# Kernel tuning notes

Hardware: AMD Instinct MI355X
Metric: run time of the kernel (lower is better)

## Reference

```python
import jax, jax.numpy as jnp
import numpy as np

B, C_IN, C_OUT, T, R, CO = 8, 64, 64, 32, 32, 32


def setup_inputs() -> dict:
    key = jax.random.key(0)
    ks = jax.random.split(key, 8)
    scale = 1.0 / np.sqrt(C_IN)  # nn.Linear default uniform(-1/sqrt(in), 1/sqrt(in))
    w = lambda k: jax.random.uniform(k, (C_OUT, C_IN), jnp.float32, -scale, scale)
    return {
        "x": jax.random.normal(ks[0], (B, C_IN, T, R, CO), jnp.float32),
        "w_self": w(ks[1]),
        "w_tp": w(ks[2]),
        "w_tm": w(ks[3]),
        "w_rp": w(ks[4]),
        "w_rm": w(ks[5]),
        "w_cp": w(ks[6]),
        "w_cm": w(ks[7]),
    }


def _proj(v, w):
    # v: [B, t, r, c, C_in], w: [C_out, C_in] (nn.Linear layout)
    return jnp.einsum('btrci,oi->btrco', v, w)


def _shift_pad(a, axis, front):
    # pad 1 slice at front (True) or back (False) along `axis` of a 5-D tensor
    pads = [(0, 0)] * 5
    pads[axis] = (1, 0) if front else (0, 1)
    return jnp.pad(a, pads)


def reference(x, w_self, w_tp, w_tm, w_rp, w_rm, w_cp, w_cm):
    xp = jnp.transpose(x, (0, 2, 3, 4, 1))  # [B, T, R, Co, C_in]
    out = _proj(xp, w_self)
    if xp.shape[1] > 1:
        out = out + _shift_pad(_proj(xp[:, :-1], w_tp), 1, True)
        out = out + _shift_pad(_proj(xp[:, 1:], w_tm), 1, False)
    if xp.shape[2] > 1:
        out = out + _shift_pad(_proj(xp[:, :, :-1], w_rp), 2, True)
        out = out + _shift_pad(_proj(xp[:, :, 1:], w_rm), 2, False)
    if xp.shape[3] > 1:
        out = out + _shift_pad(_proj(xp[:, :, :, :-1], w_cp), 3, True)
        out = out + _shift_pad(_proj(xp[:, :, :, 1:], w_cm), 3, False)
    return jnp.transpose(out, (0, 4, 1, 2, 3))  # [B, C_out, T, R, Co]
```

## Files before the change

### kernel.cpp

```cpp
#include <hip/hip_runtime.h>


#define SB 32768
#define CIN 64
#define COUT 64
#define NB 8

typedef short s16x8 __attribute__((ext_vector_type(8)));
typedef __bf16 bf16x8 __attribute__((ext_vector_type(8)));
typedef float f32x4 __attribute__((ext_vector_type(4)));

__device__ __forceinline__ unsigned f2bf(float f) {
    unsigned u = __float_as_uint(f);
    u += 0x7FFFu + ((u >> 16) & 1u);
    return u >> 16;
}
__device__ __forceinline__ unsigned pk2(float lo, float hi) {
    return f2bf(lo) | (f2bf(hi) << 16);
}

__device__ __forceinline__ void gload_lds16(const void* g, void* l) {
    __builtin_amdgcn_global_load_lds(
        (const __attribute__((address_space(1))) void*)g,
        (__attribute__((address_space(3))) void*)l, 16, 0, 0);
}

__global__ __launch_bounds__(256) void wprep_kernel(const float* __restrict__ w0,
                            const float* __restrict__ w1, const float* __restrict__ w2,
                            const float* __restrict__ w3, const float* __restrict__ w4,
                            const float* __restrict__ w5, const float* __restrict__ w6,
                            unsigned short* __restrict__ ws) {
    int tap = blockIdx.x;
    int tid = threadIdx.x;
    const float* w = (tap == 0) ? w0 : (tap == 1) ? w1 : (tap == 2) ? w2
                   : (tap == 3) ? w3 : (tap == 4) ? w4 : (tap == 5) ? w5 : w6;
    unsigned p[8];
#pragma unroll
    for (int j = 0; j < 8; ++j)
        p[j] = pk2(w[tid * 16 + 2 * j], w[tid * 16 + 2 * j + 1]);
    uint4* dp = (uint4*)(ws + tap * 4096 + tid * 16);
    dp[0] = make_uint4(p[0], p[1], p[2], p[3]);
    dp[1] = make_uint4(p[4], p[5], p[6], p[7]);
}

__global__ __launch_bounds__(256) void prep2_kernel(const float* __restrict__ x,
                            const float* __restrict__ w0, const float* __restrict__ w1,
                            const float* __restrict__ w2, const float* __restrict__ w3,
                            const float* __restrict__ w4, const float* __restrict__ w5,
                            const float* __restrict__ w6,
                            unsigned short* __restrict__ ws) {
    int bid = blockIdx.x;
    int tid = threadIdx.x;
    if (bid >= 4096) {
        int tap = bid - 4096;
        const float* w = (tap == 0) ? w0 : (tap == 1) ? w1 : (tap == 2) ? w2
                       : (tap == 3) ? w3 : (tap == 4) ? w4 : (tap == 5) ? w5 : w6;
        unsigned p[8];
#pragma unroll
        for (int j = 0; j < 8; ++j)
            p[j] = pk2(w[tid * 16 + 2 * j], w[tid * 16 + 2 * j + 1]);
        uint4* dp = (uint4*)(ws + tap * 4096 + tid * 16);
        dp[0] = make_uint4(p[0], p[1], p[2], p[3]);
        dp[1] = make_uint4(p[4], p[5], p[6], p[7]);
        return;
    }
    int lbid = ((bid & 7) << 9) | (bid >> 3);
    int b = lbid >> 9;
    int i = (lbid & 511) * 256 + tid;
    int cg = i & 7;
    int s = (i >> 3) * 2;
    const float* xb = x + (size_t)b * CIN * SB;
    unsigned short* xq = ws + 7 * 4096;
    unsigned pa[4], pb[4];
#pragma unroll
    for (int u = 0; u < 4; ++u) {
        int ch = cg * 8 + 2 * u;
        float2 v0 = *(const float2*)(xb + (size_t)ch * SB + s);
        float2 v1 = *(const float2*)(xb + (size_t)(ch + 1) * SB + s);
        pa[u] = pk2(v0.x, v1.x);
        pb[u] = pk2(v0.y, v1.y);
    }
    uint4* dst = (uint4*)(xq + ((size_t)b * SB + s) * 64 + cg * 8);
    dst[0] = make_uint4(pa[0], pa[1], pa[2], pa[3]);
    dst[8] = make_uint4(pb[0], pb[1], pb[2], pb[3]);
}

__global__ __launch_bounds__(256, 2) void conv5_kernel(const unsigned short* __restrict__ xq,
                                                       const unsigned short* __restrict__ wq,
                                                       float* __restrict__ out) {
    __shared__ uint4 alds[2560];
    int bid = blockIdx.x;
    int lbid = ((bid & 7) << 7) | (bid >> 3);
    int b = lbid >> 7;
    int sblk = (lbid & 127) << 8;
    int tid = threadIdx.x;
    int lane = tid & 63;
    int wv = tid >> 6;
    int lo = lane & 15;
    int quad = lane >> 4;
    int sbase = sblk + wv * 64;
    int t = sblk >> 10;
    const uint4* xch = (const uint4*)(xq + (size_t)b * (CIN * SB));

#pragma unroll
    for (int i = 0; i < 10; ++i) {
        int cid = wv * 640 + i * 64 + lane;
        int row = cid >> 3;
        int sc = cid & 7;
        int grow = sblk - 32 + row;
        grow = grow < 0 ? 0 : (grow > SB - 1 ? SB - 1 : grow);
        const uint4* g = xch + ((size_t)grow << 3) + (sc ^ (row & 7));
        gload_lds16((const void*)g, (void*)(alds + wv * 640 + i * 64));
    }

    int s_m[4], r_m[4], c_m[4], rl[4];
#pragma unroll
    for (int mt = 0; mt < 4; ++mt) {
        int s = sbase + mt * 16 + lo;
        s_m[mt] = s;
        r_m[mt] = (s >> 5) & 31;
        c_m[mt] = s & 31;
        rl[mt] = s - sblk + 32;
    }

    bool htm = (t > 0), htp = (t < 31);
    uint4 tgm[8], tgp[8];
    if (htm) {
#pragma unroll
        for (int ks = 0; ks < 2; ++ks)
#pragma unroll
            for (int mt = 0; mt < 4; ++mt)
                tgm[ks * 4 + mt] = xch[(size_t)(s_m[mt] - 1024) * 8 + ks * 4 + quad];
    }
    if (htp) {
#pragma unroll
        for (int ks = 0; ks < 2; ++ks)
#pragma unroll
            for (int mt = 0; mt < 4; ++mt)
                tgp[ks * 4 + mt] = xch[(size_t)(s_m[mt] + 1024) * 8 + ks * 4 + quad];
    }

    __syncthreads();

    f32x4 acc[4][4];
#pragma unroll
    for (int mt = 0; mt < 4; ++mt)
#pragma unroll
        for (int nt = 0; nt < 4; ++nt)
            acc[mt][nt] = (f32x4){0.f, 0.f, 0.f, 0.f};

    const s16x8 zz = {0, 0, 0, 0, 0, 0, 0, 0};

    auto load_b = [&](const unsigned short* wt, int ks, int nt) -> bf16x8 {
        const unsigned short* bp = wt + (nt * 16 + lo) * 64 + ks * 32 + quad * 8;
        return __builtin_bit_cast(bf16x8, *(const s16x8*)bp);
    };

    auto run_tap_reg = [&](int tap, const uint4 (&tg)[8]) {
        const unsigned short* wt = wq + tap * 4096;
        bf16x8 bf[2][4];
#pragma unroll
        for (int ks = 0; ks < 2; ++ks)
#pragma unroll
            for (int nt = 0; nt < 4; ++nt) bf[ks][nt] = load_b(wt, ks, nt);
#pragma unroll
        for (int ks = 0; ks < 2; ++ks)
#pragma unroll
            for (int mt = 0; mt < 4; ++mt) {
                bf16x8 af = __builtin_bit_cast(bf16x8, tg[ks * 4 + mt]);
#pragma unroll
                for (int nt = 0; nt < 4; ++nt)
                    acc[mt][nt] = __builtin_amdgcn_mfma_f32_16x16x32_bf16(af, bf[ks][nt], acc[mt][nt], 0, 0, 0);
            }
    };

    auto run_tap_lds = [&](int tap, int d, const bool (&ok)[4]) {
        const unsigned short* wt = wq + tap * 4096;
        bf16x8 bf[2][4];
#pragma unroll
        for (int ks = 0; ks < 2; ++ks)
#pragma unroll
            for (int nt = 0; nt < 4; ++nt) bf[ks][nt] = load_b(wt, ks, nt);
        s16x8 a[2][4];
#pragma unroll
        for (int ks = 0; ks < 2; ++ks)
#pragma unroll
            for (int mt = 0; mt < 4; ++mt) {
                int row = rl[mt] + d;
                a[ks][mt] = *((const s16x8*)alds + row * 8 + ((ks * 4 + quad) ^ (row & 7)));
            }
#pragma unroll
        for (int ks = 0; ks < 2; ++ks)
#pragma unroll
            for (int mt = 0; mt < 4; ++mt) {
                s16x8 raw = ok[mt] ? a[ks][mt] : zz;
                bf16x8 af = __builtin_bit_cast(bf16x8, raw);
#pragma unroll
                for (int nt = 0; nt < 4; ++nt)
                    acc[mt][nt] = __builtin_amdgcn_mfma_f32_16x16x32_bf16(af, bf[ks][nt], acc[mt][nt], 0, 0, 0);
            }
    };

    if (htm) run_tap_reg(1, tgm);
    if (htp) run_tap_reg(2, tgp);
    {
        bool ok_all[4] = {true, true, true, true};
        run_tap_lds(0, 0, ok_all);
    }
    {
        bool ok[4];
#pragma unroll
        for (int mt = 0; mt < 4; ++mt) ok[mt] = (r_m[mt] > 0);
        run_tap_lds(3, -32, ok);
#pragma unroll
        for (int mt = 0; mt < 4; ++mt) ok[mt] = (r_m[mt] < 31);
        run_tap_lds(4, 32, ok);
#pragma unroll
        for (int mt = 0; mt < 4; ++mt) ok[mt] = (c_m[mt] > 0);
        run_tap_lds(5, -1, ok);
#pragma unroll
        for (int mt = 0; mt < 4; ++mt) ok[mt] = (c_m[mt] < 31);
        run_tap_lds(6, 1, ok);
    }

#pragma unroll
    for (int mt = 0; mt < 4; ++mt) {
#pragma unroll
        for (int nt = 0; nt < 4; ++nt) {
            int o = nt * 16 + lo;
            size_t off = ((size_t)(b * COUT + o)) * SB + sbase + mt * 16 + quad * 4;
            *(f32x4*)(out + off) = acc[mt][nt];
        }
    }
}

__global__ __launch_bounds__(256) void conv_kernel(const float* __restrict__ x,
                                                   const unsigned short* __restrict__ wq,
                                                   float* __restrict__ out) {
    __shared__ uint4 alds[2560];
    int bid = blockIdx.x;
    int b = bid >> 7;
    int sblk = (bid & 127) << 8;
    int tid = threadIdx.x;
    const float* xb = x + (size_t)b * CIN * SB;

    {
        int rl = 32 + tid;
        const float* xp = xb + sblk + tid;
#pragma unroll
        for (int c = 0; c < 4; ++c) {
            unsigned pk[8];
#pragma unroll
            for (int u = 0; u < 8; ++u)
                pk[u] = pk2(xp[(size_t)(c * 16 + 2 * u) * SB],
                            xp[(size_t)(c * 16 + 2 * u + 1) * SB]);
            alds[rl * 8 + ((2 * c) ^ (rl & 7))] = make_uint4(pk[0], pk[1], pk[2], pk[3]);
            alds[rl * 8 + ((2 * c + 1) ^ (rl & 7))] = make_uint4(pk[4], pk[5], pk[6], pk[7]);
        }
    }
    {
        int hrow = tid & 63;
        int rl = (hrow < 32) ? hrow : hrow + 256;
        int s = sblk - 32 + rl;
        s = max(0, min(SB - 1, s));
        int ic = tid >> 6;
        const float* xp = xb + s + (size_t)(ic * 16) * SB;
        unsigned pk[8];
#pragma unroll
        for (int u = 0; u < 8; ++u)
            pk[u] = pk2(xp[(size_t)(2 * u) * SB], xp[(size_t)(2 * u + 1) * SB]);
        alds[rl * 8 + ((2 * ic) ^ (rl & 7))] = make_uint4(pk[0], pk[1], pk[2], pk[3]);
        alds[rl * 8 + ((2 * ic + 1) ^ (rl & 7))] = make_uint4(pk[4], pk[5], pk[6], pk[7]);
    }
    __syncthreads();

    int lane = tid & 63;
    int wv = tid >> 6;
    int lo = lane & 15;
    int quad = lane >> 4;
    int sbase = sblk + wv * 64;
    int t = sblk >> 10;

    f32x4 acc[4][4];
#pragma unroll
    for (int mt = 0; mt < 4; ++mt)
#pragma unroll
        for (int nt = 0; nt < 4; ++nt)
            acc[mt][nt] = (f32x4){0.f, 0.f, 0.f, 0.f};

    int r_m[4], c_m[4], rl[4];
#pragma unroll
    for (int mt = 0; mt < 4; ++mt) {
        int s = sbase + mt * 16 + lo;
        r_m[mt] = (s >> 5) & 31;
        c_m[mt] = s & 31;
        rl[mt] = s - sblk + 32;
    }

    auto load_b = [&](const unsigned short* wt, int ks, int nt) -> bf16x8 {
        const unsigned short* bp = wt + (nt * 16 + lo) * 64 + ks * 32 + quad * 8;
        return __builtin_bit_cast(bf16x8, *(const s16x8*)bp);
    };

    auto run_tap_lds = [&](int tap, int d, const bool ok[4]) {
        const unsigned short* wt = wq + tap * 4096;
#pragma unroll
        for (int ks = 0; ks < 2; ++ks) {
            bf16x8 bf[4];
#pragma unroll
            for (int nt = 0; nt < 4; ++nt) bf[nt] = load_b(wt, ks, nt);
            int j = ks * 4 + quad;
#pragma unroll
            for (int mt = 0; mt < 4; ++mt) {
                int row = rl[mt] + d;
                s16x8 raw = *((const s16x8*)alds + row * 8 + (j ^ (row & 7)));
                s16x8 zx = {0, 0, 0, 0, 0, 0, 0, 0};
                raw = ok[mt] ? raw : zx;
                bf16x8 af = __builtin_bit_cast(bf16x8, raw);
#pragma unroll
                for (int nt = 0; nt < 4; ++nt)
                    acc[mt][nt] = __builtin_amdgcn_mfma_f32_16x16x32_bf16(af, bf[nt], acc[mt][nt], 0, 0, 0);
            }
        }
    };

    auto run_tap_gather = [&](int tap, int d) {
        const unsigned short* wt = wq + tap * 4096;
#pragma unroll
        for (int ks = 0; ks < 2; ++ks) {
            bf16x8 bf[4];
#pragma unroll
            for (int nt = 0; nt < 4; ++nt) bf[nt] = load_b(wt, ks, nt);
            const float* gp = xb + (size_t)(ks * 32 + quad * 8) * SB + d;
#pragma unroll
            for (int mt = 0; mt < 4; ++mt) {
                const float* ap = gp + sbase + mt * 16 + lo;
                unsigned pk[4];
#pragma unroll
                for (int u = 0; u < 4; ++u)
                    pk[u] = pk2(ap[(size_t)(2 * u) * SB], ap[(size_t)(2 * u + 1) * SB]);
                uint4 v = make_uint4(pk[0], pk[1], pk[2], pk[3]);
                bf16x8 af = __builtin_bit_cast(bf16x8, v);
#pragma unroll
                for (int nt = 0; nt < 4; ++nt)
                    acc[mt][nt] = __builtin_amdgcn_mfma_f32_16x16x32_bf16(af, bf[nt], acc[mt][nt], 0, 0, 0);
            }
        }
    };

    {
        bool ok_all[4] = {true, true, true, true};
        run_tap_lds(0, 0, ok_all);
    }
    if (t > 0)  run_tap_gather(1, -1024);
    if (t < 31) run_tap_gather(2, 1024);
    {
        bool ok[4];
#pragma unroll
        for (int mt = 0; mt < 4; ++mt) ok[mt] = (r_m[mt] > 0);
        run_tap_lds(3, -32, ok);
#pragma unroll
        for (int mt = 0; mt < 4; ++mt) ok[mt] = (r_m[mt] < 31);
        run_tap_lds(4, 32, ok);
#pragma unroll
        for (int mt = 0; mt < 4; ++mt) ok[mt] = (c_m[mt] > 0);
        run_tap_lds(5, -1, ok);
#pragma unroll
        for (int mt = 0; mt < 4; ++mt) ok[mt] = (c_m[mt] < 31);
        run_tap_lds(6, 1, ok);
    }

#pragma unroll
    for (int mt = 0; mt < 4; ++mt) {
#pragma unroll
        for (int nt = 0; nt < 4; ++nt) {
            int o = nt * 16 + lo;
            size_t off = ((size_t)(b * COUT + o)) * SB + sbase + mt * 16 + quad * 4;
            *(f32x4*)(out + off) = acc[mt][nt];
        }
    }
}

__global__ void fallback_kernel(const float* __restrict__ x,
                                const float* __restrict__ w0, const float* __restrict__ w1,
                                const float* __restrict__ w2, const float* __restrict__ w3,
                                const float* __restrict__ w4, const float* __restrict__ w5,
                                const float* __restrict__ w6,
                                float* __restrict__ out) {
    int bid = blockIdx.x;
    int b = bid >> 11;
    int og = (bid >> 7) & 15;
    int sblk = (bid & 127) << 8;
    int tid = threadIdx.x;
    __shared__ float wl[7][4][64];
    const float* wp[7] = {w0, w1, w2, w3, w4, w5, w6};
    for (int k = tid; k < 7 * 4 * 64; k += 256) {
        int tap = k >> 8, oo = (k >> 6) & 3, i = k & 63;
        wl[tap][oo][i] = wp[tap][(og * 4 + oo) * 64 + i];
    }
    __syncthreads();
    int s = sblk + tid;
    int t = s >> 10, r = (s >> 5) & 31, c = s & 31;
    const float* xb = x + (size_t)b * CIN * SB + s;
    float a0 = 0, a1 = 0, a2 = 0, a3 = 0;
    for (int i = 0; i < 64; ++i) {
        const float* xi = xb + (size_t)i * SB;
        float vs = xi[0];
        float vtp = (t > 0) ? xi[-1024] : 0.f;
        float vtm = (t < 31) ? xi[1024] : 0.f;
        float vrp = (r > 0) ? xi[-32] : 0.f;
        float vrm = (r < 31) ? xi[32] : 0.f;
        float vcp = (c > 0) ? xi[-1] : 0.f;
        float vcm = (c < 31) ? xi[1] : 0.f;
        a0 += wl[0][0][i] * vs + wl[1][0][i] * vtp + wl[2][0][i] * vtm + wl[3][0][i] * vrp + wl[4][0][i] * vrm + wl[5][0][i] * vcp + wl[6][0][i] * vcm;
        a1 += wl[0][1][i] * vs + wl[1][1][i] * vtp + wl[2][1][i] * vtm + wl[3][1][i] * vrp + wl[4][1][i] * vrm + wl[5][1][i] * vcp + wl[6][1][i] * vcm;
        a2 += wl[0][2][i] * vs + wl[1][2][i] * vtp + wl[2][2][i] * vtm + wl[3][2][i] * vrp + wl[4][2][i] * vrm + wl[5][2][i] * vcp + wl[6][2][i] * vcm;
        a3 += wl[0][3][i] * vs + wl[1][3][i] * vtp + wl[2][3][i] * vtm + wl[3][3][i] * vrp + wl[4][3][i] * vrm + wl[5][3][i] * vcp + wl[6][3][i] * vcm;
    }
    size_t obase = ((size_t)b * COUT + og * 4) * SB + s;
    out[obase] = a0;
    out[obase + SB] = a1;
    out[obase + 2 * (size_t)SB] = a2;
    out[obase + 3 * (size_t)SB] = a3;
}

extern "C" void kernel_launch(void* const* d_in, const int* in_sizes, int n_in,
                              void* d_out, int out_size, void* d_ws, size_t ws_size,
                              hipStream_t stream) {
    const float* x = (const float*)d_in[0];
    const float* w0 = (const float*)d_in[1];
    const float* w1 = (const float*)d_in[2];
    const float* w2 = (const float*)d_in[3];
    const float* w3 = (const float*)d_in[4];
    const float* w4 = (const float*)d_in[5];
    const float* w5 = (const float*)d_in[6];
    const float* w6 = (const float*)d_in[7];
    float* out = (float*)d_out;

    size_t need_w = (size_t)7 * 4096 * 2;
    size_t need_full = need_w + (size_t)NB * CIN * SB * 2;
    if (d_ws != nullptr && ws_size >= need_full) {
        unsigned short* wsp = (unsigned short*)d_ws;
        prep2_kernel<<<4103, 256, 0, stream>>>(x, w0, w1, w2, w3, w4, w5, w6, wsp);
        conv5_kernel<<<1024, 256, 0, stream>>>(wsp + 7 * 4096, wsp, out);
    } else if (d_ws != nullptr && ws_size >= need_w) {
        unsigned short* wsp = (unsigned short*)d_ws;
        wprep_kernel<<<7, 256, 0, stream>>>(w0, w1, w2, w3, w4, w5, w6, wsp);
        conv_kernel<<<1024, 256, 0, stream>>>(x, wsp, out);
    } else {
        fallback_kernel<<<8 * 16 * 128, 256, 0, stream>>>(x, w0, w1, w2, w3, w4, w5, w6, out);
    }
}
```

Measured before the change: 169.4 us.

## Fuse prep and conv into one cooperative kernel with grid sync

Replaces the separate bf16 conversion kernel and the conv kernel with one cooperative kernel. Each block converts its own slice of x to channel-last bf16, writes it to global memory and also straight into shared memory, and blocks 0-6 convert the weights. A grid-wide barrier follows, then the block loads only the halo rows and the T-neighbour taps before running the MFMA taps. This removes a kernel launch and the re-read of the block's central tile, but it needs all 1024 blocks resident at once (launch bounds 256,4) and pays for a grid sync. If the cooperative launch fails, it falls back to the old two-kernel path.

```diff
diff --git a/kernel.cpp b/kernel.cpp
--- a/kernel.cpp
+++ b/kernel.cpp
@@ -1,4 +1,7 @@
 #include <hip/hip_runtime.h>
+#include <hip/hip_cooperative_groups.h>
+
+namespace cg = cooperative_groups;
 
 
 #define SB 32768
@@ -25,22 +28,205 @@
         (__attribute__((address_space(3))) void*)l, 16, 0, 0);
 }
 
-__global__ __launch_bounds__(256) void wprep_kernel(const float* __restrict__ w0,
-                            const float* __restrict__ w1, const float* __restrict__ w2,
-                            const float* __restrict__ w3, const float* __restrict__ w4,
-                            const float* __restrict__ w5, const float* __restrict__ w6,
-                            unsigned short* __restrict__ ws) {
-    int tap = blockIdx.x;
+__global__ __launch_bounds__(256, 4) void conv7_kernel(const float* __restrict__ x,
+        const float* __restrict__ w0, const float* __restrict__ w1,
+        const float* __restrict__ w2, const float* __restrict__ w3,
+        const float* __restrict__ w4, const float* __restrict__ w5,
+        const float* __restrict__ w6,
+        unsigned short* __restrict__ ws, float* __restrict__ out) {
+    __shared__ uint4 alds[2560];
+    int bid = blockIdx.x;
+    int lbid = ((bid & 7) << 7) | (bid >> 3);
+    int b = lbid >> 7;
+    int sblk = (lbid & 127) << 8;
     int tid = threadIdx.x;
-    const float* w = (tap == 0) ? w0 : (tap == 1) ? w1 : (tap == 2) ? w2
-                   : (tap == 3) ? w3 : (tap == 4) ? w4 : (tap == 5) ? w5 : w6;
-    unsigned p[8];
-#pragma unroll
-    for (int j = 0; j < 8; ++j)
-        p[j] = pk2(w[tid * 16 + 2 * j], w[tid * 16 + 2 * j + 1]);
-    uint4* dp = (uint4*)(ws + tap * 4096 + tid * 16);
-    dp[0] = make_uint4(p[0], p[1], p[2], p[3]);
-    dp[1] = make_uint4(p[4], p[5], p[6], p[7]);
+    unsigned short* wq = ws;
+    unsigned short* xq = ws + 7 * 4096;
+    const float* xb32 = x + (size_t)b * CIN * SB;
+    uint4* xcw = (uint4*)(xq + (size_t)b * (CIN * SB));
+
+#pragma unroll
+    for (int it = 0; it < 4; ++it) {
+        int item = it * 256 + tid;
+        int cgp = item & 7;
+        int s = sblk + (item >> 3) * 2;
+        unsigned pa[4], pb[4];
+#pragma unroll
+        for (int u = 0; u < 4; ++u) {
+            int ch = cgp * 8 + 2 * u;
+            float2 v0 = *(const float2*)(xb32 + (size_t)ch * SB + s);
+            float2 v1 = *(const float2*)(xb32 + (size_t)(ch + 1) * SB + s);
+            pa[u] = pk2(v0.x, v1.x);
+            pb[u] = pk2(v0.y, v1.y);
+        }
+        uint4 va = make_uint4(pa[0], pa[1], pa[2], pa[3]);
+        uint4 vb = make_uint4(pb[0], pb[1], pb[2], pb[3]);
+        xcw[(size_t)s * 8 + cgp] = va;
+        xcw[(size_t)(s + 1) * 8 + cgp] = vb;
+        int lr = s - sblk + 32;
+        alds[lr * 8 + (cgp ^ (lr & 7))] = va;
+        alds[(lr + 1) * 8 + (cgp ^ ((lr + 1) & 7))] = vb;
+    }
+    if (bid < 7) {
+        const float* w = (bid == 0) ? w0 : (bid == 1) ? w1 : (bid == 2) ? w2
+                       : (bid == 3) ? w3 : (bid == 4) ? w4 : (bid == 5) ? w5 : w6;
+        unsigned p[8];
+#pragma unroll
+        for (int j = 0; j < 8; ++j)
+            p[j] = pk2(w[tid * 16 + 2 * j], w[tid * 16 + 2 * j + 1]);
+        uint4* dp = (uint4*)(wq + bid * 4096 + tid * 16);
+        dp[0] = make_uint4(p[0], p[1], p[2], p[3]);
+        dp[1] = make_uint4(p[4], p[5], p[6], p[7]);
+    }
+
+    cg::this_grid().sync();
+
+    int lane = tid & 63;
+    int wv = tid >> 6;
+    int lo = lane & 15;
+    int quad = lane >> 4;
+    int sbase = sblk + wv * 64;
+    int t = sblk >> 10;
+    const uint4* xch = (const uint4*)(xq + (size_t)b * (CIN * SB));
+
+    {
+        int cid = tid;
+        int row = cid >> 3;
+        int sc = cid & 7;
+        int grow = sblk - 32 + row;
+        grow = grow < 0 ? 0 : grow;
+        gload_lds16((const void*)(xch + ((size_t)grow << 3) + (sc ^ (row & 7))),
+                    (void*)(alds + wv * 64));
+    }
+    {
+        int cid = tid;
+        int row = (cid >> 3) + 288;
+        int sc = cid & 7;
+        int grow = sblk - 32 + row;
+        grow = grow > SB - 1 ? SB - 1 : grow;
+        gload_lds16((const void*)(xch + ((size_t)grow << 3) + (sc ^ (row & 7))),
+                    (void*)(alds + 2304 + wv * 64));
+    }
+
+    int s_m[4], r_m[4], c_m[4], rl[4];
+#pragma unroll
+    for (int mt = 0; mt < 4; ++mt) {
+        int s = sbase + mt * 16 + lo;
+        s_m[mt] = s;
+        r_m[mt] = (s >> 5) & 31;
+        c_m[mt] = s & 31;
+        rl[mt] = s - sblk + 32;
+    }
+
+    bool htm = (t > 0), htp = (t < 31);
+    uint4 tgm[8], tgp[8];
+    if (htm) {
+#pragma unroll
+        for (int ks = 0; ks < 2; ++ks)
+#pragma unroll
+            for (int mt = 0; mt < 4; ++mt)
+                tgm[ks * 4 + mt] = xch[(size_t)(s_m[mt] - 1024) * 8 + ks * 4 + quad];
+    }
+    if (htp) {
+#pragma unroll
+        for (int ks = 0; ks < 2; ++ks)
+#pragma unroll
+            for (int mt = 0; mt < 4; ++mt)
+                tgp[ks * 4 + mt] = xch[(size_t)(s_m[mt] + 1024) * 8 + ks * 4 + quad];
+    }
+
+    __syncthreads();
+
+    f32x4 acc[4][4];
+#pragma unroll
+    for (int mt = 0; mt < 4; ++mt)
+#pragma unroll
+        for (int nt = 0; nt < 4; ++nt)
+            acc[mt][nt] = (f32x4){0.f, 0.f, 0.f, 0.f};
+
+    const s16x8 zz = {0, 0, 0, 0, 0, 0, 0, 0};
+
+    auto load_b = [&](const unsigned short* wt, int ks, int nt) -> bf16x8 {
+        const unsigned short* bp = wt + (nt * 16 + lo) * 64 + ks * 32 + quad * 8;
+        return __builtin_bit_cast(bf16x8, *(const s16x8*)bp);
+    };
+
+    auto run_tap_reg = [&](int tap, const uint4 (&tg)[8]) {
+        const unsigned short* wt = wq + tap * 4096;
+        bf16x8 bf[2][4];
+#pragma unroll
+        for (int ks = 0; ks < 2; ++ks)
+#pragma unroll
+            for (int nt = 0; nt < 4; ++nt) bf[ks][nt] = load_b(wt, ks, nt);
+#pragma unroll
+        for (int ks = 0; ks < 2; ++ks)
+#pragma unroll
+            for (int mt = 0; mt < 4; ++mt) {
+                bf16x8 af = __builtin_bit_cast(bf16x8, tg[ks * 4 + mt]);
+#pragma unroll
+                for (int nt = 0; nt < 4; ++nt)
+                    acc[mt][nt] = __builtin_amdgcn_mfma_f32_16x16x32_bf16(af, bf[ks][nt], acc[mt][nt], 0, 0, 0);
+            }
+    };
+
+    auto run_tap_lds = [&](int tap, int d, const bool (&ok)[4]) {
+        const unsigned short* wt = wq + tap * 4096;
+        bf16x8 bf[2][4];
+#pragma unroll
+        for (int ks = 0; ks < 2; ++ks)
+#pragma unroll
+            for (int nt = 0; nt < 4; ++nt) bf[ks][nt] = load_b(wt, ks, nt);
+        s16x8 a[2][4];
+#pragma unroll
+        for (int ks = 0; ks < 2; ++ks)
+#pragma unroll
+            for (int mt = 0; mt < 4; ++mt) {
+                int row = rl[mt] + d;
+                a[ks][mt] = *((const s16x8*)alds + row * 8 + ((ks * 4 + quad) ^ (row & 7)));
+            }
+#pragma unroll
+        for (int ks = 0; ks < 2; ++ks)
+#pragma unroll
+            for (int mt = 0; mt < 4; ++mt) {
+                s16x8 raw = ok[mt] ? a[ks][mt] : zz;
+                bf16x8 af = __builtin_bit_cast(bf16x8, raw);
+#pragma unroll
+                for (int nt = 0; nt < 4; ++nt)
+                    acc[mt][nt] = __builtin_amdgcn_mfma_f32_16x16x32_bf16(af, bf[ks][nt], acc[mt][nt], 0, 0, 0);
+            }
+    };
+
+    if (htm) run_tap_reg(1, tgm);
+    if (htp) run_tap_reg(2, tgp);
+    {
+        bool ok_all[4] = {true, true, true, true};
+        run_tap_lds(0, 0, ok_all);
+    }
+    {
+        bool ok[4];
+#pragma unroll
+        for (int mt = 0; mt < 4; ++mt) ok[mt] = (r_m[mt] > 0);
+        run_tap_lds(3, -32, ok);
+#pragma unroll
+        for (int mt = 0; mt < 4; ++mt) ok[mt] = (r_m[mt] < 31);
+        run_tap_lds(4, 32, ok);
+#pragma unroll
+        for (int mt = 0; mt < 4; ++mt) ok[mt] = (c_m[mt] > 0);
+        run_tap_lds(5, -1, ok);
+#pragma unroll
+        for (int mt = 0; mt < 4; ++mt) ok[mt] = (c_m[mt] < 31);
+        run_tap_lds(6, 1, ok);
+    }
+
+#pragma unroll
+    for (int mt = 0; mt < 4; ++mt) {
+#pragma unroll
+        for (int nt = 0; nt < 4; ++nt) {
+            int o = nt * 16 + lo;
+            size_t off = ((size_t)(b * COUT + o)) * SB + sbase + mt * 16 + quad * 4;
+            *(f32x4*)(out + off) = acc[mt][nt];
+        }
+    }
 }
 
 __global__ __launch_bounds__(256) void prep2_kernel(const float* __restrict__ x,
@@ -67,20 +253,20 @@
     int lbid = ((bid & 7) << 9) | (bid >> 3);
     int b = lbid >> 9;
     int i = (lbid & 511) * 256 + tid;
-    int cg = i & 7;
+    int cgp = i & 7;
     int s = (i >> 3) * 2;
     const float* xb = x + (size_t)b * CIN * SB;
     unsigned short* xq = ws + 7 * 4096;
     unsigned pa[4], pb[4];
 #pragma unroll
     for (int u = 0; u < 4; ++u) {
-        int ch = cg * 8 + 2 * u;
+        int ch = cgp * 8 + 2 * u;
         float2 v0 = *(const float2*)(xb + (size_t)ch * SB + s);
         float2 v1 = *(const float2*)(xb + (size_t)(ch + 1) * SB + s);
         pa[u] = pk2(v0.x, v1.x);
         pb[u] = pk2(v0.y, v1.y);
     }
-    uint4* dst = (uint4*)(xq + ((size_t)b * SB + s) * 64 + cg * 8);
+    uint4* dst = (uint4*)(xq + ((size_t)b * SB + s) * 64 + cgp * 8);
     dst[0] = make_uint4(pa[0], pa[1], pa[2], pa[3]);
     dst[8] = make_uint4(pb[0], pb[1], pb[2], pb[3]);
 }
@@ -232,6 +418,24 @@
             *(f32x4*)(out + off) = acc[mt][nt];
         }
     }
+}
+
+__global__ __launch_bounds__(256) void wprep_kernel(const float* __restrict__ w0,
+                            const float* __restrict__ w1, const float* __restrict__ w2,
+                            const float* __restrict__ w3, const float* __restrict__ w4,
+                            const float* __restrict__ w5, const float* __restrict__ w6,
+                            unsigned short* __restrict__ ws) {
+    int tap = blockIdx.x;
+    int tid = threadIdx.x;
+    const float* w = (tap == 0) ? w0 : (tap == 1) ? w1 : (tap == 2) ? w2
+                   : (tap == 3) ? w3 : (tap == 4) ? w4 : (tap == 5) ? w5 : w6;
+    unsigned p[8];
+#pragma unroll
+    for (int j = 0; j < 8; ++j)
+        p[j] = pk2(w[tid * 16 + 2 * j], w[tid * 16 + 2 * j + 1]);
+    uint4* dp = (uint4*)(ws + tap * 4096 + tid * 16);
+    dp[0] = make_uint4(p[0], p[1], p[2], p[3]);
+    dp[1] = make_uint4(p[4], p[5], p[6], p[7]);
 }
 
 __global__ __launch_bounds__(256) void conv_kernel(const float* __restrict__ x,
@@ -441,8 +645,14 @@
     size_t need_full = need_w + (size_t)NB * CIN * SB * 2;
     if (d_ws != nullptr && ws_size >= need_full) {
         unsigned short* wsp = (unsigned short*)d_ws;
-        prep2_kernel<<<4103, 256, 0, stream>>>(x, w0, w1, w2, w3, w4, w5, w6, wsp);
-        conv5_kernel<<<1024, 256, 0, stream>>>(wsp + 7 * 4096, wsp, out);
+        void* kargs[] = {(void*)&x, (void*)&w0, (void*)&w1, (void*)&w2, (void*)&w3,
+                         (void*)&w4, (void*)&w5, (void*)&w6, (void*)&wsp, (void*)&out};
+        hipError_t ce = hipLaunchCooperativeKernel((const void*)conv7_kernel,
+                                                   dim3(1024), dim3(256), kargs, 0, stream);
+        if (ce != hipSuccess) {
+            prep2_kernel<<<4103, 256, 0, stream>>>(x, w0, w1, w2, w3, w4, w5, w6, wsp);
+            conv5_kernel<<<1024, 256, 0, stream>>>(wsp + 7 * 4096, wsp, out);
+        }
     } else if (d_ws != nullptr && ws_size >= need_w) {
         unsigned short* wsp = (unsigned short*)d_ws;
         wprep_kernel<<<7, 256, 0, stream>>>(w0, w1, w2, w3, w4, w5, w6, wsp);
```

Result: slower. 378.1 us (+123.2%).
